# Optimization experiments

Measured on AMD Instinct MI355X. Metric: run time of the kernel, lower is better.

## Reference

```python
import jax, jax.numpy as jnp
import numpy as np

GROUPS = 32
HEADS = 8
EPS = 1e-5

def setup_inputs() -> dict:
    key = jax.random.key(0)
    ks = jax.random.split(key, 5)
    C = 512
    x = jax.random.normal(ks[0], (8, C, 32, 32), dtype=jnp.float32)
    gn_w = jnp.ones((C,), dtype=jnp.float32)
    gn_b = jnp.zeros((C,), dtype=jnp.float32)
    qkv_w = jax.random.normal(ks[1], (3 * C, C), dtype=jnp.float32) * 0.02
    qkv_b = jnp.zeros((3 * C,), dtype=jnp.float32)
    proj_w = jax.random.normal(ks[2], (C, C), dtype=jnp.float32) * 0.02
    proj_b = jnp.zeros((C,), dtype=jnp.float32)
    return {"x": x, "gn_w": gn_w, "gn_b": gn_b, "qkv_w": qkv_w,
            "qkv_b": qkv_b, "proj_w": proj_w, "proj_b": proj_b}

def reference(x, gn_w, gn_b, qkv_w, qkv_b, proj_w, proj_b):
    B, C, H, W = x.shape
    d = C // HEADS
    # GroupNorm(32, C)
    xg = x.reshape(B, GROUPS, C // GROUPS, H, W)
    mean = xg.mean(axis=(2, 3, 4), keepdims=True)
    var = xg.var(axis=(2, 3, 4), keepdims=True)
    h = ((xg - mean) * jax.lax.rsqrt(var + EPS)).reshape(B, C, H, W)
    h = h * gn_w[None, :, None, None] + gn_b[None, :, None, None]
    # 1x1 conv QKV == channel matmul
    qkv = jnp.einsum('bchw,oc->bohw', h, qkv_w) + qkv_b[None, :, None, None]
    qkv = qkv.reshape(B, 3, HEADS, d, H * W)
    q, k, v = qkv[:, 0], qkv[:, 1], qkv[:, 2]  # [B, heads, d, HW]
    scale = d ** (-0.5)
    # weight[b,h,q,k] = sum_d q[b,h,d,q] * k[b,h,d,k] * scale
    attn = jax.nn.softmax(jnp.einsum('bhdq,bhdk->bhqk', q, k) * scale, axis=-1)
    # out[b,h,d,q] = sum_k v[b,h,d,k] * attn[b,h,q,k]
    out = jnp.einsum('bhdk,bhqk->bhdq', v, attn).reshape(B, C, H, W)
    out = jnp.einsum('bchw,oc->bohw', out, proj_w) + proj_b[None, :, None, None]
    return out + x
```

## Files before the change

### kernel.cpp

```cpp
#include <hip/hip_runtime.h>
#include <math.h>

#define B_    8
#define C_    512
#define HW_   1024
#define O3_   1536
#define HEADS_ 8
#define D_    64
#define G_    32
#define CPG_  16
#define EPS_  1e-5f
#define M_TOT 8192

#define QSCALE (0.125f * 1.44269504088896f)

typedef __bf16 bf16x8 __attribute__((ext_vector_type(8)));
typedef __bf16 bf16x4 __attribute__((ext_vector_type(4)));
typedef float  f32x4  __attribute__((ext_vector_type(4)));

__device__ __forceinline__ void async_copy16(void* lds, const void* g) {
  __builtin_amdgcn_global_load_lds(
      (const __attribute__((address_space(1))) unsigned int*)g,
      (__attribute__((address_space(3))) unsigned int*)lds, 16, 0, 0);
}

__global__ __launch_bounds__(256) void k_gn(const float* __restrict__ x,
                                            const float* __restrict__ gw,
                                            const float* __restrict__ gb,
                                            __bf16* __restrict__ h,
                                            const float* __restrict__ qw,
                                            const float* __restrict__ pw,
                                            __bf16* __restrict__ qwb,
                                            __bf16* __restrict__ pwb) {
  __shared__ float red[10];
  __shared__ float X[16 * 1024];
  __shared__ __bf16 T[16 * 1032];
  if (blockIdx.x >= B_ * G_) {
    int nconv = 256;
    int i0 = (blockIdx.x - B_ * G_) * 256 + threadIdx.x;
    for (int i = i0; i < O3_ * C_ / 4; i += nconv * 256) {
      float4 v = ((const float4*)qw)[i];
      bf16x4 o = {(__bf16)v.x, (__bf16)v.y, (__bf16)v.z, (__bf16)v.w};
      ((bf16x4*)qwb)[i] = o;
    }
    for (int i = i0; i < C_ * C_ / 4; i += nconv * 256) {
      float4 v = ((const float4*)pw)[i];
      bf16x4 o = {(__bf16)v.x, (__bf16)v.y, (__bf16)v.z, (__bf16)v.w};
      ((bf16x4*)pwb)[i] = o;
    }
    return;
  }
  int bg = blockIdx.x;
  int b = bg >> 5, g = bg & 31;
  const float4* xg4 = (const float4*)(x + ((size_t)(b * C_) + g * CPG_) * HW_);
  int tid = threadIdx.x;

  float s = 0.f, ss = 0.f;
  for (int i = tid; i < CPG_ * HW_ / 4; i += 256) {
    float4 v = xg4[i];
    ((float4*)X)[i] = v;
    s += v.x + v.y + v.z + v.w;
    ss += v.x * v.x + v.y * v.y + v.z * v.z + v.w * v.w;
  }
  for (int off = 32; off > 0; off >>= 1) {
    s  += __shfl_down(s, off, 64);
    ss += __shfl_down(ss, off, 64);
  }
  int wv = tid >> 6;
  if ((tid & 63) == 0) { red[wv] = s; red[4 + wv] = ss; }
  __syncthreads();
  if (tid == 0) {
    float S  = red[0] + red[1] + red[2] + red[3];
    float SS = red[4] + red[5] + red[6] + red[7];
    float mean = S / (float)(CPG_ * HW_);
    float var  = SS / (float)(CPG_ * HW_) - mean * mean;
    red[8] = mean;
    red[9] = rsqrtf(var + EPS_);
  }
  __syncthreads();
  float mean = red[8], rstd = red[9];

  for (int i = tid; i < CPG_ * HW_ / 4; i += 256) {
    int c = i >> 8;
    int hw4 = (i & 255) * 4;
    float ga = gw[g * CPG_ + c], be = gb[g * CPG_ + c];
    float4 v = ((const float4*)X)[i];
    bf16x4 pk;
    pk[0] = (__bf16)((v.x - mean) * rstd * ga + be);
    pk[1] = (__bf16)((v.y - mean) * rstd * ga + be);
    pk[2] = (__bf16)((v.z - mean) * rstd * ga + be);
    pk[3] = (__bf16)((v.w - mean) * rstd * ga + be);
    *(bf16x4*)(&T[c * 1032 + hw4]) = pk;
  }
  __syncthreads();

  __bf16* hb = h + (size_t)b * HW_ * C_ + g * CPG_;
  for (int j = tid; j < 2 * HW_; j += 256) {
    int hw = j >> 1, c8 = (j & 1) * 8;
    bf16x8 v;
#pragma unroll
    for (int jj = 0; jj < 8; jj++) v[jj] = T[(c8 + jj) * 1032 + hw];
    *(bf16x8*)(hb + (size_t)hw * C_ + c8) = v;
  }
}

#define BK 64
__global__ __launch_bounds__(256) void k_qkv(const __bf16* __restrict__ h,
                                             const __bf16* __restrict__ w,
                                             const float* __restrict__ bias,
                                             __bf16* __restrict__ y,
                                             __bf16* __restrict__ vT) {
  __shared__ __align__(16) __bf16 As[2][128 * BK];
  __shared__ __align__(16) __bf16 Bs[2][128 * BK];
  int m0 = blockIdx.x * 128, n0 = blockIdx.y * 128;
  int t = threadIdx.x;
  int lane = t & 63, l16 = lane & 15, quad = lane >> 4;
  int wv = t >> 6;
  int wm = (wv >> 1) * 64, wn = (wv & 1) * 64;

  int rsub = lane >> 3;
  int chunk = (lane & 7) ^ rsub;
  const __bf16* ag = h + (size_t)(m0 + wv * 32 + rsub) * C_ + chunk * 8;
  const __bf16* bg = w + (size_t)(n0 + wv * 32 + rsub) * C_ + chunk * 8;
  int sw = l16 & 7;

  auto stage = [&](int k0, int bi) {
    __bf16* la = As[bi] + wv * 2048 + lane * 8;
    __bf16* lb = Bs[bi] + wv * 2048 + lane * 8;
#pragma unroll
    for (int s = 0; s < 4; s++) {
      async_copy16(la + s * 512, ag + (size_t)(s * 8) * C_ + k0);
      async_copy16(lb + s * 512, bg + (size_t)(s * 8) * C_ + k0);
    }
  };

  f32x4 acc[4][4];
#pragma unroll
  for (int i = 0; i < 4; i++)
#pragma unroll
    for (int j = 0; j < 4; j++) acc[i][j] = f32x4{0.f, 0.f, 0.f, 0.f};

  stage(0, 0);
  for (int kk = 0; kk < 8; kk++) {
    int bi = kk & 1;
    asm volatile("s_waitcnt vmcnt(0)\n\ts_barrier" ::: "memory");
    if (kk < 7) stage((kk + 1) * BK, bi ^ 1);
    const __bf16* as = As[bi];
    const __bf16* bs = Bs[bi];
#pragma unroll
    for (int hh = 0; hh < 2; hh++) {
      bf16x8 af[4], bf[4];
#pragma unroll
      for (int i = 0; i < 4; i++) {
        af[i] = *(const bf16x8*)(as + (wm + i * 16 + l16) * BK +
                                 ((hh * 4 + quad) ^ sw) * 8);
        bf[i] = *(const bf16x8*)(bs + (wn + i * 16 + l16) * BK +
                                 ((hh * 4 + quad) ^ sw) * 8);
      }
#pragma unroll
      for (int i = 0; i < 4; i++)
#pragma unroll
        for (int j = 0; j < 4; j++)
          acc[i][j] = __builtin_amdgcn_mfma_f32_16x16x32_bf16(af[i], bf[j],
                                                              acc[i][j], 0, 0, 0);
    }
  }

  if (n0 >= 2 * C_) {
    int bb = m0 >> 10;
    int tokBase = (m0 & 1023) + wm + quad * 4;
#pragma unroll
    for (int j = 0; j < 4; j++) {
      int n = n0 + wn + j * 16 + l16;
      int c = n - 2 * C_;
      float bv = bias[n];
      __bf16* vrow = vT + ((size_t)(bb * C_) + c) * HW_;
#pragma unroll
      for (int i = 0; i < 4; i++) {
        bf16x4 pk;
#pragma unroll
        for (int r = 0; r < 4; r++) pk[r] = (__bf16)(acc[i][j][r] + bv);
        *(bf16x4*)(vrow + tokBase + i * 16) = pk;
      }
    }
  } else {
    float sc = (n0 < C_) ? QSCALE : 1.0f;
#pragma unroll
    for (int j = 0; j < 4; j++) {
      int n = n0 + wn + j * 16 + l16;
      float bv = bias[n];
#pragma unroll
      for (int i = 0; i < 4; i++)
#pragma unroll
        for (int r = 0; r < 4; r++) {
          int m = m0 + wm + i * 16 + quad * 4 + r;
          y[(size_t)m * O3_ + n] = (__bf16)((acc[i][j][r] + bv) * sc);
        }
    }
  }
}

__global__ __launch_bounds__(256) void k_attn(const __bf16* __restrict__ y,
                                              const __bf16* __restrict__ vT,
                                              __bf16* __restrict__ ao) {
  __shared__ __align__(16) __bf16 Ks[2][128 * 64];
  __shared__ __align__(16) __bf16 Vt[2][64 * 128];
  __shared__ __align__(16) __bf16 Pp[4][32 * 36];
  int hd = blockIdx.x, b = blockIdx.y, qt = blockIdx.z;
  int t = threadIdx.x;
  int wv = t >> 6, lane = t & 63, l16 = lane & 15, quad = lane >> 4;
  int q0 = qt * 128 + wv * 32;

  const __bf16* base = y + (size_t)(b * HW_) * O3_ + hd * D_;
  const __bf16* kg = base + C_;
  const __bf16* vtg = vT + ((size_t)(b * C_) + hd * D_) * HW_;

  bf16x8 qb[2][2];
#pragma unroll
  for (int qg = 0; qg < 2; qg++)
#pragma unroll
    for (int dh = 0; dh < 2; dh++)
      qb[qg][dh] = *(const bf16x8*)(base + (size_t)(q0 + qg * 16 + l16) * O3_ +
                                    dh * 32 + quad * 8);

  int kRowSub = lane >> 3;
  int kChunk = (lane & 7) ^ (kRowSub & 7);

  auto stage = [&](int kt, int bi) {
#pragma unroll
    for (int s = 0; s < 4; s++) {
      int row = wv * 32 + s * 8 + kRowSub;
      async_copy16(&Ks[bi][(wv * 32 + s * 8) * 64 + lane * 8],
                   kg + (size_t)(kt + row) * O3_ + kChunk * 8);
    }
#pragma unroll
    for (int s = 0; s < 4; s++) {
      int row = wv * 16 + s * 4 + (lane >> 4);
      int c2 = (lane & 15) ^ (row & 15);
      async_copy16(&Vt[bi][(wv * 16 + s * 4) * 128 + lane * 8],
                   vtg + (size_t)row * HW_ + kt + c2 * 8);
    }
  };

  float l_run[2] = {0.f, 0.f};
  f32x4 o_acc[4][2];
#pragma unroll
  for (int dt = 0; dt < 4; dt++)
#pragma unroll
    for (int qg = 0; qg < 2; qg++) o_acc[dt][qg] = f32x4{0.f, 0.f, 0.f, 0.f};

  stage(0, 0);

  for (int step = 0; step < 8; step++) {
    int bi = step & 1;
    asm volatile("s_waitcnt vmcnt(0)\n\ts_barrier" ::: "memory");
    if (step < 7) stage((step + 1) * 128, bi ^ 1);

    const __bf16* ks = Ks[bi];
    const __bf16* vs = Vt[bi];
#pragma unroll
    for (int kh = 0; kh < 4; kh++) {
      f32x4 st[2][2];
#pragma unroll
      for (int tti = 0; tti < 2; tti++) {
        int row = (kh * 2 + tti) * 16 + l16;
        bf16x8 ka0 = *(const bf16x8*)(&ks[row * 64 + ((quad) ^ (l16 & 7)) * 8]);
        bf16x8 ka1 = *(const bf16x8*)(&ks[row * 64 + ((4 + quad) ^ (l16 & 7)) * 8]);
        f32x4 z = {0.f, 0.f, 0.f, 0.f};
        st[tti][0] = __builtin_amdgcn_mfma_f32_16x16x32_bf16(ka0, qb[0][0], z, 0, 0, 0);
        st[tti][0] = __builtin_amdgcn_mfma_f32_16x16x32_bf16(ka1, qb[0][1], st[tti][0], 0, 0, 0);
        st[tti][1] = __builtin_amdgcn_mfma_f32_16x16x32_bf16(ka0, qb[1][0], z, 0, 0, 0);
        st[tti][1] = __builtin_amdgcn_mfma_f32_16x16x32_bf16(ka1, qb[1][1], st[tti][1], 0, 0, 0);
      }
#pragma unroll
      for (int qg = 0; qg < 2; qg++) {
        float rs = 0.f;
#pragma unroll
        for (int tti = 0; tti < 2; tti++)
#pragma unroll
          for (int r = 0; r < 4; r++) {
            float e = __builtin_amdgcn_exp2f(st[tti][qg][r]);
            st[tti][qg][r] = e;
            rs += e;
          }
        l_run[qg] += rs;
      }
#pragma unroll
      for (int qg = 0; qg < 2; qg++)
#pragma unroll
        for (int tti = 0; tti < 2; tti++) {
          bf16x4 pk;
#pragma unroll
          for (int r = 0; r < 4; r++) pk[r] = (__bf16)st[tti][qg][r];
          *(bf16x4*)(&Pp[wv][(qg * 16 + l16) * 36 + tti * 16 + quad * 4]) = pk;
        }
      asm volatile("s_waitcnt lgkmcnt(0)" ::: "memory");
      bf16x8 pb0 = *(const bf16x8*)(&Pp[wv][l16 * 36 + quad * 8]);
      bf16x8 pb1 = *(const bf16x8*)(&Pp[wv][(16 + l16) * 36 + quad * 8]);
#pragma unroll
      for (int dt = 0; dt < 4; dt++) {
        int vpos = ((kh * 4 + quad) ^ l16) * 8;
        bf16x8 va = *(const bf16x8*)(&vs[(dt * 16 + l16) * 128 + vpos]);
        o_acc[dt][0] = __builtin_amdgcn_mfma_f32_16x16x32_bf16(va, pb0, o_acc[dt][0], 0, 0, 0);
        o_acc[dt][1] = __builtin_amdgcn_mfma_f32_16x16x32_bf16(va, pb1, o_acc[dt][1], 0, 0, 0);
      }
    }
  }

#pragma unroll
  for (int qg = 0; qg < 2; qg++) {
    l_run[qg] += __shfl_xor(l_run[qg], 16, 64);
    l_run[qg] += __shfl_xor(l_run[qg], 32, 64);
  }
  float inv0 = 1.f / l_run[0], inv1 = 1.f / l_run[1];

#pragma unroll
  for (int dt = 0; dt < 4; dt++) {
    bf16x4 p0, p1;
#pragma unroll
    for (int r = 0; r < 4; r++) {
      p0[r] = (__bf16)(o_acc[dt][0][r] * inv0);
      p1[r] = (__bf16)(o_acc[dt][1][r] * inv1);
    }
    int ch = hd * D_ + dt * 16 + quad * 4;
    *(bf16x4*)(ao + (size_t)(b * HW_ + q0 + l16) * C_ + ch) = p0;
    *(bf16x4*)(ao + (size_t)(b * HW_ + q0 + 16 + l16) * C_ + ch) = p1;
  }
}

__global__ __launch_bounds__(256) void k_proj(const __bf16* __restrict__ ao,
                                              const __bf16* __restrict__ w,
                                              const float* __restrict__ bias,
                                              const float* __restrict__ x,
                                              float* __restrict__ out) {
  __shared__ __align__(16) __bf16 As[2][128 * BK];
  __shared__ __align__(16) __bf16 Bs[2][64 * BK];
  int n0 = blockIdx.x * 64, m0 = blockIdx.y * 128;
  int t = threadIdx.x;
  int lane = t & 63, l16 = lane & 15, quad = lane >> 4;
  int wv = t >> 6;
  int wm = (wv >> 1) * 64, wn = (wv & 1) * 32;

  int rsub = lane >> 3;
  int chunk = (lane & 7) ^ rsub;
  const __bf16* ag = w + (size_t)(m0 + wv * 32 + rsub) * C_ + chunk * 8;
  const __bf16* bg = ao + (size_t)(n0 + wv * 16 + rsub) * C_ + chunk * 8;
  int sw = l16 & 7;

  auto stage = [&](int k0, int bi) {
    __bf16* la = As[bi] + wv * 2048 + lane * 8;
    __bf16* lb = Bs[bi] + wv * 1024 + lane * 8;
#pragma unroll
    for (int s = 0; s < 4; s++)
      async_copy16(la + s * 512, ag + (size_t)(s * 8) * C_ + k0);
#pragma unroll
    for (int s = 0; s < 2; s++)
      async_copy16(lb + s * 512, bg + (size_t)(s * 8) * C_ + k0);
  };

  f32x4 acc[4][2];
#pragma unroll
  for (int i = 0; i < 4; i++)
#pragma unroll
    for (int j = 0; j < 2; j++) acc[i][j] = f32x4{0.f, 0.f, 0.f, 0.f};

  stage(0, 0);
  for (int kk = 0; kk < 8; kk++) {
    int bi = kk & 1;
    asm volatile("s_waitcnt vmcnt(0)\n\ts_barrier" ::: "memory");
    if (kk < 7) stage((kk + 1) * BK, bi ^ 1);
    const __bf16* as = As[bi];
    const __bf16* bs = Bs[bi];
#pragma unroll
    for (int hh = 0; hh < 2; hh++) {
      bf16x8 af[4], bf[2];
#pragma unroll
      for (int i = 0; i < 4; i++)
        af[i] = *(const bf16x8*)(as + (wm + i * 16 + l16) * BK +
                                 ((hh * 4 + quad) ^ sw) * 8);
#pragma unroll
      for (int j = 0; j < 2; j++)
        bf[j] = *(const bf16x8*)(bs + (wn + j * 16 + l16) * BK +
                                 ((hh * 4 + quad) ^ sw) * 8);
#pragma unroll
      for (int i = 0; i < 4; i++)
#pragma unroll
        for (int j = 0; j < 2; j++)
          acc[i][j] = __builtin_amdgcn_mfma_f32_16x16x32_bf16(af[i], bf[j],
                                                              acc[i][j], 0, 0, 0);
    }
  }

  int bb = n0 >> 10;
#pragma unroll
  for (int i = 0; i < 4; i++)
#pragma unroll
    for (int r = 0; r < 4; r++) {
      int o = m0 + wm + i * 16 + quad * 4 + r;
      float bv = bias[o];
#pragma unroll
      for (int j = 0; j < 2; j++) {
        int n = n0 + wn + j * 16 + l16;
        int hw = n & 1023;
        size_t idx = ((size_t)(bb * C_ + o)) * HW_ + hw;
        out[idx] = acc[i][j][r] + bv + x[idx];
      }
    }
}

extern "C" void kernel_launch(void* const* d_in, const int* in_sizes, int n_in,
                              void* d_out, int out_size, void* d_ws, size_t ws_size,
                              hipStream_t stream) {
  const float* x      = (const float*)d_in[0];
  const float* gn_w   = (const float*)d_in[1];
  const float* gn_b   = (const float*)d_in[2];
  const float* qkv_w  = (const float*)d_in[3];
  const float* qkv_b  = (const float*)d_in[4];
  const float* proj_w = (const float*)d_in[5];
  const float* proj_b = (const float*)d_in[6];
  float* out = (float*)d_out;

  char* ws = (char*)d_ws;
  __bf16* h   = (__bf16*)(ws);
  __bf16* qwb = (__bf16*)(ws + 8388608);
  __bf16* pwb = (__bf16*)(ws + 8388608 + 1572864);
  __bf16* yq  = (__bf16*)(ws + 8388608 + 1572864 + 524288);
  __bf16* ao  = (__bf16*)(ws + 8388608 + 1572864 + 524288 + 25165824);
  __bf16* vT  = (__bf16*)(ws + 8388608 + 1572864 + 524288 + 25165824 + 8388608);

  k_gn  <<<B_ * G_ + 256, 256, 0, stream>>>(x, gn_w, gn_b, h,
                                            qkv_w, proj_w, qwb, pwb);
  k_qkv <<<dim3(M_TOT / 128, O3_ / 128, 1), 256, 0, stream>>>(h, qwb, qkv_b, yq, vT);
  k_attn<<<dim3(HEADS_, B_, 8), 256, 0, stream>>>(yq, vT, ao);
  k_proj<<<dim3(M_TOT / 64, C_ / 128, 1), 256, 0, stream>>>(ao, pwb, proj_b, x, out);
  (void)in_sizes; (void)n_in; (void)out_size; (void)ws_size;
}
```

Before: 152.9 us.

## Widen GroupNorm blocks, shrink QKV K-tile for occupancy, add MFMA priority hints

The GroupNorm kernel now uses 1024-thread blocks and drops the 64 KB fp32 LDS staging buffer, re-reading x from global memory for the normalize pass. The weight-conversion tail uses fewer, larger blocks. The QKV GEMM halves its K tile to 32 with a matching swizzle and adds a 3-blocks-per-CU launch bound, cutting LDS per block so more blocks can be resident, at the cost of twice as many barrier iterations. The attention kernel wraps its MFMA sections in s_setprio to favour matrix issue across waves.

```diff
diff --git a/kernel.cpp b/kernel.cpp
--- a/kernel.cpp
+++ b/kernel.cpp
@@ -24,26 +24,25 @@
       (__attribute__((address_space(3))) unsigned int*)lds, 16, 0, 0);
 }
 
-__global__ __launch_bounds__(256) void k_gn(const float* __restrict__ x,
-                                            const float* __restrict__ gw,
-                                            const float* __restrict__ gb,
-                                            __bf16* __restrict__ h,
-                                            const float* __restrict__ qw,
-                                            const float* __restrict__ pw,
-                                            __bf16* __restrict__ qwb,
-                                            __bf16* __restrict__ pwb) {
-  __shared__ float red[10];
-  __shared__ float X[16 * 1024];
+__global__ __launch_bounds__(1024) void k_gn(const float* __restrict__ x,
+                                             const float* __restrict__ gw,
+                                             const float* __restrict__ gb,
+                                             __bf16* __restrict__ h,
+                                             const float* __restrict__ qw,
+                                             const float* __restrict__ pw,
+                                             __bf16* __restrict__ qwb,
+                                             __bf16* __restrict__ pwb) {
+  __shared__ float red[34];
   __shared__ __bf16 T[16 * 1032];
+  int tid = threadIdx.x;
   if (blockIdx.x >= B_ * G_) {
-    int nconv = 256;
-    int i0 = (blockIdx.x - B_ * G_) * 256 + threadIdx.x;
-    for (int i = i0; i < O3_ * C_ / 4; i += nconv * 256) {
+    int i0 = (blockIdx.x - B_ * G_) * 1024 + tid;
+    for (int i = i0; i < O3_ * C_ / 4; i += 64 * 1024) {
       float4 v = ((const float4*)qw)[i];
       bf16x4 o = {(__bf16)v.x, (__bf16)v.y, (__bf16)v.z, (__bf16)v.w};
       ((bf16x4*)qwb)[i] = o;
     }
-    for (int i = i0; i < C_ * C_ / 4; i += nconv * 256) {
+    for (int i = i0; i < C_ * C_ / 4; i += 64 * 1024) {
       float4 v = ((const float4*)pw)[i];
       bf16x4 o = {(__bf16)v.x, (__bf16)v.y, (__bf16)v.z, (__bf16)v.w};
       ((bf16x4*)pwb)[i] = o;
@@ -53,12 +52,10 @@
   int bg = blockIdx.x;
   int b = bg >> 5, g = bg & 31;
   const float4* xg4 = (const float4*)(x + ((size_t)(b * C_) + g * CPG_) * HW_);
-  int tid = threadIdx.x;
 
   float s = 0.f, ss = 0.f;
-  for (int i = tid; i < CPG_ * HW_ / 4; i += 256) {
+  for (int i = tid; i < CPG_ * HW_ / 4; i += 1024) {
     float4 v = xg4[i];
-    ((float4*)X)[i] = v;
     s += v.x + v.y + v.z + v.w;
     ss += v.x * v.x + v.y * v.y + v.z * v.z + v.w * v.w;
   }
@@ -67,24 +64,25 @@
     ss += __shfl_down(ss, off, 64);
   }
   int wv = tid >> 6;
-  if ((tid & 63) == 0) { red[wv] = s; red[4 + wv] = ss; }
+  if ((tid & 63) == 0) { red[wv] = s; red[16 + wv] = ss; }
   __syncthreads();
   if (tid == 0) {
-    float S  = red[0] + red[1] + red[2] + red[3];
-    float SS = red[4] + red[5] + red[6] + red[7];
+    float S = 0.f, SS = 0.f;
+#pragma unroll
+    for (int i = 0; i < 16; i++) { S += red[i]; SS += red[16 + i]; }
     float mean = S / (float)(CPG_ * HW_);
     float var  = SS / (float)(CPG_ * HW_) - mean * mean;
-    red[8] = mean;
-    red[9] = rsqrtf(var + EPS_);
+    red[32] = mean;
+    red[33] = rsqrtf(var + EPS_);
   }
   __syncthreads();
-  float mean = red[8], rstd = red[9];
-
-  for (int i = tid; i < CPG_ * HW_ / 4; i += 256) {
+  float mean = red[32], rstd = red[33];
+
+  for (int i = tid; i < CPG_ * HW_ / 4; i += 1024) {
     int c = i >> 8;
     int hw4 = (i & 255) * 4;
     float ga = gw[g * CPG_ + c], be = gb[g * CPG_ + c];
-    float4 v = ((const float4*)X)[i];
+    float4 v = xg4[i];
     bf16x4 pk;
     pk[0] = (__bf16)((v.x - mean) * rstd * ga + be);
     pk[1] = (__bf16)((v.y - mean) * rstd * ga + be);
@@ -95,7 +93,7 @@
   __syncthreads();
 
   __bf16* hb = h + (size_t)b * HW_ * C_ + g * CPG_;
-  for (int j = tid; j < 2 * HW_; j += 256) {
+  for (int j = tid; j < 2 * HW_; j += 1024) {
     int hw = j >> 1, c8 = (j & 1) * 8;
     bf16x8 v;
 #pragma unroll
@@ -104,33 +102,33 @@
   }
 }
 
-#define BK 64
-__global__ __launch_bounds__(256) void k_qkv(const __bf16* __restrict__ h,
-                                             const __bf16* __restrict__ w,
-                                             const float* __restrict__ bias,
-                                             __bf16* __restrict__ y,
-                                             __bf16* __restrict__ vT) {
-  __shared__ __align__(16) __bf16 As[2][128 * BK];
-  __shared__ __align__(16) __bf16 Bs[2][128 * BK];
+#define BKQ 32
+__global__ __launch_bounds__(256, 3) void k_qkv(const __bf16* __restrict__ h,
+                                                const __bf16* __restrict__ w,
+                                                const float* __restrict__ bias,
+                                                __bf16* __restrict__ y,
+                                                __bf16* __restrict__ vT) {
+  __shared__ __align__(16) __bf16 As[2][128 * BKQ];
+  __shared__ __align__(16) __bf16 Bs[2][128 * BKQ];
   int m0 = blockIdx.x * 128, n0 = blockIdx.y * 128;
   int t = threadIdx.x;
   int lane = t & 63, l16 = lane & 15, quad = lane >> 4;
   int wv = t >> 6;
   int wm = (wv >> 1) * 64, wn = (wv & 1) * 64;
 
-  int rsub = lane >> 3;
-  int chunk = (lane & 7) ^ rsub;
+  int rsub = lane >> 2;
+  int chunk = (lane & 3) ^ (rsub & 3);
   const __bf16* ag = h + (size_t)(m0 + wv * 32 + rsub) * C_ + chunk * 8;
   const __bf16* bg = w + (size_t)(n0 + wv * 32 + rsub) * C_ + chunk * 8;
-  int sw = l16 & 7;
+  int sw = l16 & 3;
 
   auto stage = [&](int k0, int bi) {
-    __bf16* la = As[bi] + wv * 2048 + lane * 8;
-    __bf16* lb = Bs[bi] + wv * 2048 + lane * 8;
-#pragma unroll
-    for (int s = 0; s < 4; s++) {
-      async_copy16(la + s * 512, ag + (size_t)(s * 8) * C_ + k0);
-      async_copy16(lb + s * 512, bg + (size_t)(s * 8) * C_ + k0);
+    __bf16* la = As[bi] + wv * 1024 + lane * 8;
+    __bf16* lb = Bs[bi] + wv * 1024 + lane * 8;
+#pragma unroll
+    for (int s = 0; s < 2; s++) {
+      async_copy16(la + s * 512, ag + (size_t)(s * 16) * C_ + k0);
+      async_copy16(lb + s * 512, bg + (size_t)(s * 16) * C_ + k0);
     }
   };
 
@@ -141,29 +139,24 @@
     for (int j = 0; j < 4; j++) acc[i][j] = f32x4{0.f, 0.f, 0.f, 0.f};
 
   stage(0, 0);
-  for (int kk = 0; kk < 8; kk++) {
+  for (int kk = 0; kk < 16; kk++) {
     int bi = kk & 1;
     asm volatile("s_waitcnt vmcnt(0)\n\ts_barrier" ::: "memory");
-    if (kk < 7) stage((kk + 1) * BK, bi ^ 1);
+    if (kk < 15) stage((kk + 1) * BKQ, bi ^ 1);
     const __bf16* as = As[bi];
     const __bf16* bs = Bs[bi];
-#pragma unroll
-    for (int hh = 0; hh < 2; hh++) {
-      bf16x8 af[4], bf[4];
-#pragma unroll
-      for (int i = 0; i < 4; i++) {
-        af[i] = *(const bf16x8*)(as + (wm + i * 16 + l16) * BK +
-                                 ((hh * 4 + quad) ^ sw) * 8);
-        bf[i] = *(const bf16x8*)(bs + (wn + i * 16 + l16) * BK +
-                                 ((hh * 4 + quad) ^ sw) * 8);
-      }
-#pragma unroll
-      for (int i = 0; i < 4; i++)
-#pragma unroll
-        for (int j = 0; j < 4; j++)
-          acc[i][j] = __builtin_amdgcn_mfma_f32_16x16x32_bf16(af[i], bf[j],
-                                                              acc[i][j], 0, 0, 0);
-    }
+    bf16x8 af[4], bf[4];
+#pragma unroll
+    for (int i = 0; i < 4; i++) {
+      af[i] = *(const bf16x8*)(as + (wm + i * 16 + l16) * BKQ + (quad ^ sw) * 8);
+      bf[i] = *(const bf16x8*)(bs + (wn + i * 16 + l16) * BKQ + (quad ^ sw) * 8);
+    }
+#pragma unroll
+    for (int i = 0; i < 4; i++)
+#pragma unroll
+      for (int j = 0; j < 4; j++)
+        acc[i][j] = __builtin_amdgcn_mfma_f32_16x16x32_bf16(af[i], bf[j],
+                                                            acc[i][j], 0, 0, 0);
   }
 
   if (n0 >= 2 * C_) {
@@ -261,6 +254,7 @@
 #pragma unroll
     for (int kh = 0; kh < 4; kh++) {
       f32x4 st[2][2];
+      __builtin_amdgcn_s_setprio(1);
 #pragma unroll
       for (int tti = 0; tti < 2; tti++) {
         int row = (kh * 2 + tti) * 16 + l16;
@@ -272,6 +266,7 @@
         st[tti][1] = __builtin_amdgcn_mfma_f32_16x16x32_bf16(ka0, qb[1][0], z, 0, 0, 0);
         st[tti][1] = __builtin_amdgcn_mfma_f32_16x16x32_bf16(ka1, qb[1][1], st[tti][1], 0, 0, 0);
       }
+      __builtin_amdgcn_s_setprio(0);
 #pragma unroll
       for (int qg = 0; qg < 2; qg++) {
         float rs = 0.f;
@@ -297,6 +292,7 @@
       asm volatile("s_waitcnt lgkmcnt(0)" ::: "memory");
       bf16x8 pb0 = *(const bf16x8*)(&Pp[wv][l16 * 36 + quad * 8]);
       bf16x8 pb1 = *(const bf16x8*)(&Pp[wv][(16 + l16) * 36 + quad * 8]);
+      __builtin_amdgcn_s_setprio(1);
 #pragma unroll
       for (int dt = 0; dt < 4; dt++) {
         int vpos = ((kh * 4 + quad) ^ l16) * 8;
@@ -304,6 +300,7 @@
         o_acc[dt][0] = __builtin_amdgcn_mfma_f32_16x16x32_bf16(va, pb0, o_acc[dt][0], 0, 0, 0);
         o_acc[dt][1] = __builtin_amdgcn_mfma_f32_16x16x32_bf16(va, pb1, o_acc[dt][1], 0, 0, 0);
       }
+      __builtin_amdgcn_s_setprio(0);
     }
   }
 
@@ -328,6 +325,7 @@
   }
 }
 
+#define BK 64
 __global__ __launch_bounds__(256) void k_proj(const __bf16* __restrict__ ao,
                                               const __bf16* __restrict__ w,
                                               const float* __restrict__ bias,
@@ -428,7 +426,7 @@
   __bf16* ao  = (__bf16*)(ws + 8388608 + 1572864 + 524288 + 25165824);
   __bf16* vT  = (__bf16*)(ws + 8388608 + 1572864 + 524288 + 25165824 + 8388608);
 
-  k_gn  <<<B_ * G_ + 256, 256, 0, stream>>>(x, gn_w, gn_b, h,
+  k_gn  <<<B_ * G_ + 64, 1024, 0, stream>>>(x, gn_w, gn_b, h,
                                             qkv_w, proj_w, qwb, pwb);
   k_qkv <<<dim3(M_TOT / 128, O3_ / 128, 1), 256, 0, stream>>>(h, qwb, qkv_b, yq, vT);
   k_attn<<<dim3(HEADS_, B_, 8), 256, 0, stream>>>(yq, vT, ao);
```

Measured after the change: 144.7 us. -5.4%, faster.
